# Kernel optimization log

Measured on AMD Instinct MI355X. Metric: run time of the kernel, lower is better.

## Reference

```python
import jax, jax.numpy as jnp
import numpy as np

NUM_CLASSES = 81
THRESHOLD = 0.5
NEGPOS_RATIO = 3
VARIANCE = (0.1, 0.2)


def point_form(p):
    # center-size -> corner form
    return jnp.concatenate([p[:, :2] - p[:, 2:] / 2, p[:, :2] + p[:, 2:] / 2], axis=1)


def jaccard(box_a, box_b):
    # box_a: [O,4] corners, box_b: [P,4] corners -> IoU [O,P]
    lt = jnp.maximum(box_a[:, None, :2], box_b[None, :, :2])
    rb = jnp.minimum(box_a[:, None, 2:], box_b[None, :, 2:])
    wh = jnp.clip(rb - lt, 0.0)
    inter = wh[..., 0] * wh[..., 1]
    area_a = ((box_a[:, 2] - box_a[:, 0]) * (box_a[:, 3] - box_a[:, 1]))[:, None]
    area_b = ((box_b[:, 2] - box_b[:, 0]) * (box_b[:, 3] - box_b[:, 1]))[None, :]
    return inter / (area_a + area_b - inter)


def encode(matched, priors, variances):
    # matched: [P,4] corner GT, priors: [P,4] center-size
    g_cxcy = (matched[:, :2] + matched[:, 2:]) / 2 - priors[:, :2]
    g_cxcy = g_cxcy / (variances[0] * priors[:, 2:])
    g_wh = (matched[:, 2:] - matched[:, :2]) / priors[:, 2:]
    g_wh = jnp.log(g_wh) / variances[1]
    return jnp.concatenate([g_cxcy, g_wh], axis=1)


def match_one(truths, labels, priors):
    overlaps = jaccard(truths, point_form(priors))   # [O,P]
    best_prior_idx = jnp.argmax(overlaps, axis=1)     # [O] best prior per truth
    best_truth_overlap = jnp.max(overlaps, axis=0)    # [P]
    best_truth_idx = jnp.argmax(overlaps, axis=0)     # [P] best truth per prior
    # force each truth's best prior to match that truth
    best_truth_overlap = best_truth_overlap.at[best_prior_idx].set(2.0)
    best_truth_idx = best_truth_idx.at[best_prior_idx].set(jnp.arange(truths.shape[0]))
    matched = truths[best_truth_idx]                  # [P,4]
    conf = labels[best_truth_idx].astype(jnp.int32) + 1
    conf = jnp.where(best_truth_overlap < THRESHOLD, 0, conf)
    loc = encode(matched, priors, VARIANCE)
    return loc, conf


def _loss(loc_data, conf_data, targets, priors):
    B, P, C = conf_data.shape
    loc_t, conf_t = jax.vmap(lambda t: match_one(t[:, :4], t[:, 4], priors))(targets)
    pos = conf_t > 0                                  # [B,P]
    # smooth-L1 (beta=1) over positive priors, sum reduction
    d = loc_data - loc_t
    sl1 = jnp.where(jnp.abs(d) < 1.0, 0.5 * d * d, jnp.abs(d) - 0.5)
    loss_l = jnp.sum(jnp.where(pos[..., None], sl1, 0.0))
    # per-prior CE used both for mining ranking and the final conf loss
    ce = jax.nn.logsumexp(conf_data, axis=-1) - jnp.take_along_axis(
        conf_data, conf_t[..., None], axis=-1)[..., 0]   # [B,P]
    # hard negative mining: zero positives, double argsort for rank
    loss_c_rank = jnp.where(pos, 0.0, ce)
    loss_idx = jnp.argsort(-loss_c_rank, axis=1)
    idx_rank = jnp.argsort(loss_idx, axis=1)
    num_pos = jnp.sum(pos, axis=1, keepdims=True)     # [B,1]
    num_neg = jnp.minimum(NEGPOS_RATIO * num_pos, P - 1)
    neg = idx_rank < num_neg
    sel = pos | neg
    loss_c = jnp.sum(jnp.where(sel, ce, 0.0))
    N = jnp.sum(num_pos).astype(loc_data.dtype)
    return loss_l / N, loss_c / N


def setup_inputs():
    key = jax.random.key(0)
    kl, kc, kb1, kb2, kll, kp1, kp2 = jax.random.split(key, 7)
    B, P, O, C = 64, 8732, 50, NUM_CLASSES
    loc_data = jax.random.normal(kl, (B, P, 4), jnp.float32)
    conf_data = jax.random.normal(kc, (B, P, C), jnp.float32)
    # valid GT boxes in corner form inside [0,1]
    cxcy = jax.random.uniform(kb1, (B, O, 2), minval=0.2, maxval=0.8)
    wh = jax.random.uniform(kb2, (B, O, 2), minval=0.05, maxval=0.3)
    boxes = jnp.concatenate([cxcy - wh / 2, cxcy + wh / 2], axis=-1)
    labels = jax.random.randint(kll, (B, O), 0, C - 1).astype(jnp.float32)
    targets = jnp.concatenate([boxes, labels[..., None]], axis=-1)  # [B,O,5]
    # priors in center-size form
    pcxcy = jax.random.uniform(kp1, (P, 2), minval=0.05, maxval=0.95)
    pwh = jax.random.uniform(kp2, (P, 2), minval=0.05, maxval=0.5)
    priors = jnp.concatenate([pcxcy, pwh], axis=-1)
    return {"loc_data": loc_data, "conf_data": conf_data, "targets": targets, "priors": priors}


def reference(loc_data, conf_data, targets, priors):
    return _loss(loc_data, conf_data, targets, priors)
```

## Files before the change

kernel.cpp:

```cpp
#include <hip/hip_runtime.h>
#include <float.h>

#pragma clang fp contract(off)

typedef unsigned long long ull;
typedef unsigned int u32;

#define THRESH 0.5f
#define PPT 4
#define CE_R 128
#define SEL_T 512
#define ENC_SEG 1024


__device__ __forceinline__ float sl1(float d) {
    float a = fabsf(d);
    return (a < 1.f) ? 0.5f * d * d : a - 0.5f;
}

__global__ __launch_bounds__(256) void k_match(
        const float* __restrict__ targets, const float* __restrict__ priors,
        float* __restrict__ bto, int* __restrict__ bti, int P, int O, int SEG) {
    const int b = blockIdx.y, seg = blockIdx.x;
    __shared__ float4 tbox[128];
    __shared__ float tarea[128];
    const float* trow = targets + (size_t)b * O * 5;
    for (int o = threadIdx.x; o < O; o += blockDim.x) {
        float x1 = trow[o * 5 + 0], y1 = trow[o * 5 + 1];
        float x2 = trow[o * 5 + 2], y2 = trow[o * 5 + 3];
        tbox[o] = make_float4(x1, y1, x2, y2);
        tarea[o] = (x2 - x1) * (y2 - y1);
    }
    __syncthreads();
    const int p0 = seg * SEG;
    float px1[PPT], py1[PPT], px2[PPT], py2[PPT], pa[PPT];
    float bestv[PPT]; int besto[PPT]; int pidx[PPT];
#pragma unroll
    for (int j = 0; j < PPT; j++) {
        int p = p0 + (int)threadIdx.x + j * 256;
        pidx[j] = p; bestv[j] = -1.f; besto[j] = 0;
        if (p < P) {
            float4 pr = ((const float4*)priors)[p];
            px1[j] = pr.x - pr.z / 2.f;
            py1[j] = pr.y - pr.w / 2.f;
            px2[j] = pr.x + pr.z / 2.f;
            py2[j] = pr.y + pr.w / 2.f;
            pa[j] = (px2[j] - px1[j]) * (py2[j] - py1[j]);
        } else {
            px1[j] = 2.f; py1[j] = 2.f; px2[j] = 2.f; py2[j] = 2.f; pa[j] = 1.f;
        }
    }
    for (int o = 0; o < O; o++) {
        float4 t = tbox[o];
        float ta = tarea[o];
#pragma unroll
        for (int j = 0; j < PPT; j++) {
            float lx = fmaxf(t.x, px1[j]), ly = fmaxf(t.y, py1[j]);
            float rx = fminf(t.z, px2[j]), ry = fminf(t.w, py2[j]);
            float wx = fmaxf(rx - lx, 0.f), wy = fmaxf(ry - ly, 0.f);
            float inter = wx * wy;
            float iou = 0.f;
            if (inter > 0.f) iou = inter / (ta + pa[j] - inter);
            if (iou > bestv[j]) { bestv[j] = iou; besto[j] = o; }
        }
    }
#pragma unroll
    for (int j = 0; j < PPT; j++) {
        if (pidx[j] < P) {
            bto[(size_t)b * P + pidx[j]] = bestv[j];
            bti[(size_t)b * P + pidx[j]] = besto[j];
        }
    }
}

__global__ __launch_bounds__(256) void k_tbest(
        const float* __restrict__ targets, const float* __restrict__ priors,
        ull* __restrict__ tbest, int P, int O, int npairs) {
    int g = blockIdx.x * 4 + ((int)threadIdx.x >> 6);
    int lane = threadIdx.x & 63;
    if (g >= npairs) return;
    int OP = (O + 1) >> 1;
    int b = g / OP;
    int o0 = (g % OP) * 2;
    const float* trow = targets + ((size_t)b * O + o0) * 5;
    float ax1 = trow[0], ay1 = trow[1], ax2 = trow[2], ay2 = trow[3];
    float ta0 = (ax2 - ax1) * (ay2 - ay1);
    bool has1 = (o0 + 1) < O;
    float cx1 = 0, cy1 = 0, cx2 = 0, cy2 = 0, ta1 = 1.f;
    if (has1) {
        cx1 = trow[5]; cy1 = trow[6]; cx2 = trow[7]; cy2 = trow[8];
        ta1 = (cx2 - cx1) * (cy2 - cy1);
    }
    ull k0 = 0, k1 = 0;
    for (int p = lane; p < P; p += 64) {
        float4 pr = ((const float4*)priors)[p];
        float bx1 = pr.x - pr.z / 2.f;
        float by1 = pr.y - pr.w / 2.f;
        float bx2 = pr.x + pr.z / 2.f;
        float by2 = pr.y + pr.w / 2.f;
        float pa = (bx2 - bx1) * (by2 - by1);
        u32 np = ~(u32)p;
        {
            float lx = fmaxf(ax1, bx1), ly = fmaxf(ay1, by1);
            float rx = fminf(ax2, bx2), ry = fminf(ay2, by2);
            float wx = fmaxf(rx - lx, 0.f), wy = fmaxf(ry - ly, 0.f);
            float inter = wx * wy;
            float iou = 0.f;
            if (inter > 0.f) iou = inter / (ta0 + pa - inter);
            ull key = ((ull)__float_as_uint(iou) << 32) | np;
            if (key > k0) k0 = key;
        }
        if (has1) {
            float lx = fmaxf(cx1, bx1), ly = fmaxf(cy1, by1);
            float rx = fminf(cx2, bx2), ry = fminf(cy2, by2);
            float wx = fmaxf(rx - lx, 0.f), wy = fmaxf(ry - ly, 0.f);
            float inter = wx * wy;
            float iou = 0.f;
            if (inter > 0.f) iou = inter / (ta1 + pa - inter);
            ull key = ((ull)__float_as_uint(iou) << 32) | np;
            if (key > k1) k1 = key;
        }
    }
    for (int off = 32; off; off >>= 1) {
        ull a = __shfl_xor(k0, off); if (a > k0) k0 = a;
        ull d = __shfl_xor(k1, off); if (d > k1) k1 = d;
    }
    if (lane == 0) {
        tbest[(size_t)b * O + o0] = k0;
        if (has1) tbest[(size_t)b * O + o0 + 1] = k1;
    }
}

__global__ __launch_bounds__(256) void k_encode(
        const float* __restrict__ targets, const float* __restrict__ priors,
        const float* __restrict__ loc_data, const ull* __restrict__ tbest,
        const float* __restrict__ bto, int* __restrict__ conf_t,
        int* __restrict__ num_pos, float* __restrict__ loss_l,
        int P, int O, int SEG) {
    const int b = blockIdx.y, seg = blockIdx.x;
    __shared__ float tr[64 * 5];
    __shared__ int ov[ENC_SEG];
    __shared__ float redf[4]; __shared__ int redi[4];
    const int p0 = seg * SEG;
    const int p1 = min(p0 + SEG, P);
    const float* trow = targets + (size_t)b * O * 5;
    for (int i = threadIdx.x; i < O * 5; i += blockDim.x) tr[i] = trow[i];
    for (int i = threadIdx.x; i < p1 - p0; i += blockDim.x) ov[i] = -1;
    __syncthreads();
    if ((int)threadIdx.x < O) {
        ull tb = tbest[(size_t)b * O + threadIdx.x];
        u32 p = ~(u32)(tb & 0xFFFFFFFFULL);
        if (p >= (u32)P) p = 0;
        if ((int)p >= p0 && (int)p < p1) atomicMax(&ov[p - p0], (int)threadIdx.x);
    }
    __syncthreads();
    float ll = 0.f; int cnt = 0;
    for (int p = p0 + (int)threadIdx.x; p < p1; p += blockDim.x) {
        size_t idx = (size_t)b * P + p;
        int o = conf_t[idx];
        int ovv = ov[p - p0];
        bool forced = ovv >= 0;
        if (forced) o = ovv;
        float ovl = bto[idx];
        int conf = (!forced && ovl < THRESH) ? 0 : ((int)tr[o * 5 + 4] + 1);
        conf_t[idx] = conf;
        if (conf > 0) {
            cnt++;
            float4 pr = ((const float4*)priors)[p];
            float mx1 = tr[o * 5], my1 = tr[o * 5 + 1];
            float mx2 = tr[o * 5 + 2], my2 = tr[o * 5 + 3];
            float gx = ((mx1 + mx2) / 2.f - pr.x) / (0.1f * pr.z);
            float gy = ((my1 + my2) / 2.f - pr.y) / (0.1f * pr.w);
            float gw = logf((mx2 - mx1) / pr.z) / 0.2f;
            float gh = logf((my2 - my1) / pr.w) / 0.2f;
            float4 ld = ((const float4*)loc_data)[idx];
            ll += sl1(ld.x - gx) + sl1(ld.y - gy) + sl1(ld.z - gw) + sl1(ld.w - gh);
        }
    }
    for (int off = 32; off; off >>= 1) {
        ll += __shfl_down(ll, off);
        cnt += __shfl_down(cnt, off);
    }
    int w = threadIdx.x >> 6;
    if ((threadIdx.x & 63) == 0) { redf[w] = ll; redi[w] = cnt; }
    __syncthreads();
    if (threadIdx.x == 0) {
        float l = 0; int c = 0;
        for (int i = 0; i < 4; i++) { l += redf[i]; c += redi[i]; }
        if (c) atomicAdd(&num_pos[b], c);
        atomicAdd(&loss_l[b], l);
    }
}

__global__ __launch_bounds__(256) void k_ce(
        const float* __restrict__ conf, const int* __restrict__ conf_t,
        float* __restrict__ ce, long long BP) {
    __shared__ float s[CE_R * 81];
    long long r0 = (long long)blockIdx.x * CE_R;
    int nrow = (int)min((long long)CE_R, BP - r0);
    int nfl = nrow * 81;
    const float* src = conf + r0 * 81;
    int nv4 = nfl >> 2;
    const float4* s4 = (const float4*)src;
    for (int i = threadIdx.x; i < nv4; i += 256)
        ((float4*)s)[i] = s4[i];
    for (int i = (nv4 << 2) + (int)threadIdx.x; i < nfl; i += 256)
        s[i] = src[i];
    __syncthreads();
    int row = threadIdx.x >> 1;
    int half = threadIdx.x & 1;
    if (row < nrow) {
        const float* rp = s + row * 81;
        int c0 = half * 41;
        int cn = half ? 40 : 41;
        float sum = 0.f;
        for (int j = 0; j < cn; j++) sum += __expf(rp[c0 + j]);
        sum += __shfl_xor(sum, 1);
        if (half == 0) {
            long long r = r0 + row;
            int t = conf_t[r];
            ce[r] = __logf(sum) - rp[t];
        }
    }
}

__global__ __launch_bounds__(SEL_T) void k_select(
        const float* __restrict__ ce, const int* __restrict__ conf_t,
        const int* __restrict__ num_pos, const float* __restrict__ loss_l,
        float* __restrict__ acc, u32* __restrict__ ticket,
        float* __restrict__ out, int P, int B) {
    extern __shared__ u32 sk[];
    __shared__ u32 whist[SEL_T / 64][16];
    __shared__ u32 hist[16];
    __shared__ float redf[SEL_T / 64]; __shared__ u32 redu[SEL_T / 64];
    __shared__ u32 sh_pval; __shared__ int sh_rem;
    const int b = blockIdx.x;
    const size_t base = (size_t)b * P;
    const int lane = threadIdx.x & 63;
    const int w = threadIdx.x >> 6;
    const int NW = SEL_T / 64;

    float ps = 0.f;
    for (int p = threadIdx.x; p < P; p += SEL_T) {
        int c = conf_t[base + p];
        float v = ce[base + p];
        u32 key;
        if (c > 0) { ps += v; key = 0u; }
        else key = __float_as_uint(fmaxf(v, 0.f));
        sk[p] = key;
    }
    for (int off = 32; off; off >>= 1) ps += __shfl_down(ps, off);
    if (lane == 0) redf[w] = ps;
    __syncthreads();
    float pos_sum = 0.f;
    if (threadIdx.x == 0) {
        for (int i = 0; i < NW; i++) pos_sum += redf[i];
    }

    const int np = num_pos[b];
    const int k = min(3 * np, P - 1);
    u32 pval = 0, pmask = 0; int rem = k;
    if (k > 0) {
        for (int shift = 28; shift >= 0; shift -= 4) {
            __syncthreads();
            ull a0 = 0, a1 = 0;
            for (int p = threadIdx.x; p < P; p += SEL_T) {
                u32 key = sk[p];
                if ((key & pmask) == pval) {
                    u32 dig = (key >> shift) & 15u;
                    ull inc = 1ull << ((dig & 7u) * 8u);
                    if (dig < 8u) a0 += inc; else a1 += inc;
                }
            }
            const ull M = 0x00FF00FF00FF00FFull;
            ull e0 = a0 & M, e1 = (a0 >> 8) & M, e2 = a1 & M, e3 = (a1 >> 8) & M;
            for (int off = 32; off; off >>= 1) {
                e0 += __shfl_xor(e0, off);
                e1 += __shfl_xor(e1, off);
                e2 += __shfl_xor(e2, off);
                e3 += __shfl_xor(e3, off);
            }
            if (lane == 0) {
#pragma unroll
                for (int j = 0; j < 4; j++) {
                    whist[w][2 * j]     = (u32)((e0 >> (16 * j)) & 0xFFFF);
                    whist[w][2 * j + 1] = (u32)((e1 >> (16 * j)) & 0xFFFF);
                    whist[w][8 + 2 * j]     = (u32)((e2 >> (16 * j)) & 0xFFFF);
                    whist[w][8 + 2 * j + 1] = (u32)((e3 >> (16 * j)) & 0xFFFF);
                }
            }
            __syncthreads();
            if (threadIdx.x < 16) {
                u32 h = 0;
                for (int i = 0; i < NW; i++) h += whist[i][threadIdx.x];
                hist[threadIdx.x] = h;
            }
            __syncthreads();
            if (threadIdx.x == 0) {
                u32 accu = 0; int d = 15;
                for (; d > 0; d--) {
                    u32 h = hist[d];
                    if (accu + h >= (u32)rem) break;
                    accu += h;
                }
                sh_pval = pval | ((u32)d << shift);
                sh_rem = rem - (int)accu;
            }
            __syncthreads();
            pval = sh_pval; rem = sh_rem; pmask |= (0xFu << shift);
        }
    }

    float sgt = 0.f; u32 cgt = 0;
    if (k > 0) {
        for (int p = threadIdx.x; p < P; p += SEL_T) {
            u32 key = sk[p];
            if (key > pval) { sgt += __uint_as_float(key); cgt++; }
        }
    }
    for (int off = 32; off; off >>= 1) {
        sgt += __shfl_down(sgt, off);
        cgt += __shfl_down(cgt, off);
    }
    __syncthreads();
    if (lane == 0) { redf[w] = sgt; redu[w] = cgt; }
    __syncthreads();
    if (threadIdx.x == 0) {
        float s = 0.f; u32 c = 0;
        for (int i = 0; i < NW; i++) { s += redf[i]; c += redu[i]; }
        float t = __uint_as_float(pval);
        float lc_b = pos_sum + ((k > 0) ? (s + (float)(k - (int)c) * t) : 0.f);
        atomicAdd(&acc[0], (float)np);
        atomicAdd(&acc[1], loss_l[b]);
        atomicAdd(&acc[2], lc_b);
        __threadfence();
        u32 tk = atomicAdd(ticket, 1u);
        if (tk == (u32)(B - 1)) {
            float n  = atomicAdd(&acc[0], 0.f);
            float ll = atomicAdd(&acc[1], 0.f);
            float lc = atomicAdd(&acc[2], 0.f);
            out[0] = ll / n;
            out[1] = lc / n;
        }
    }
}


extern "C" void kernel_launch(void* const* d_in, const int* in_sizes, int n_in,
                              void* d_out, int out_size, void* d_ws, size_t ws_size,
                              hipStream_t stream) {
    const float* loc     = (const float*)d_in[0];
    const float* conf    = (const float*)d_in[1];
    const float* targets = (const float*)d_in[2];
    const float* priors  = (const float*)d_in[3];

    const int P = in_sizes[3] / 4;
    const int B = in_sizes[0] / (P * 4);
    const int O = in_sizes[2] / (B * 5);

    char* ws = (char*)d_ws;
    size_t off = 0;
    int*   num_pos = (int*)(ws + off);   off += (size_t)B * sizeof(int);
    float* loss_l  = (float*)(ws + off); off += (size_t)B * sizeof(float);
    float* acc     = (float*)(ws + off); off += 4 * sizeof(float);
    u32*   ticket  = (u32*)(ws + off);   off += sizeof(u32);
    const size_t zbytes = off;
    off = (off + 7) & ~(size_t)7;
    ull*   tbest   = (ull*)(ws + off);   off += (size_t)B * O * sizeof(ull);
    float* F       = (float*)(ws + off); off += (size_t)B * P * sizeof(float);
    int*   I       = (int*)(ws + off);   off += (size_t)B * P * sizeof(int);

    (void)hipMemsetAsync(d_ws, 0, zbytes, stream);

    const int SEG = 256 * PPT;
    const int S = (P + SEG - 1) / SEG;
    k_match<<<dim3(S, B), 256, 0, stream>>>(targets, priors, F, I, P, O, SEG);

    const int npairs = B * ((O + 1) / 2);
    k_tbest<<<(npairs + 3) / 4, 256, 0, stream>>>(targets, priors, tbest, P, O, npairs);

    const int S2 = (P + ENC_SEG - 1) / ENC_SEG;
    const int SEG2 = (P + S2 - 1) / S2;
    k_encode<<<dim3(S2, B), 256, 0, stream>>>(targets, priors, loc, tbest, F, I,
                                              num_pos, loss_l, P, O, SEG2);

    const long long BP = (long long)B * P;
    k_ce<<<(int)((BP + CE_R - 1) / CE_R), 256, 0, stream>>>(conf, I, F, BP);

    k_select<<<B, SEL_T, (size_t)P * sizeof(u32), stream>>>(F, I, num_pos, loss_l,
                                                            acc, ticket, (float*)d_out, P, B);
}
```

Before: 402.8 us.

## Fuse match/tbest kernels and encode/CE kernels, drop memset launch

Merges the per-prior match and per-truth best-prior kernels into one launch partitioned by block index, and folds the workspace zeroing into block 0 instead of a separate memset. Encode and cross-entropy are fused so each block computes conf_t into shared memory and then streams its slice of conf_data to compute CE, avoiding a re-read of conf_t and two launches. The fused CE block now uses much more shared memory (about 41KB+8KB), which may reduce occupancy for the bandwidth-heavy conf_data pass. There is also a fixed ENC_SEG segmentation with fewer blocks (9x64) doing CE versus many small blocks before.

```diff
diff --git a/kernel.cpp b/kernel.cpp
--- a/kernel.cpp
+++ b/kernel.cpp
@@ -18,134 +18,142 @@
     return (a < 1.f) ? 0.5f * d * d : a - 0.5f;
 }
 
-__global__ __launch_bounds__(256) void k_match(
+__global__ __launch_bounds__(256) void k_prep(
         const float* __restrict__ targets, const float* __restrict__ priors,
-        float* __restrict__ bto, int* __restrict__ bti, int P, int O, int SEG) {
-    const int b = blockIdx.y, seg = blockIdx.x;
+        float* __restrict__ bto, int* __restrict__ bti, ull* __restrict__ tbest,
+        u32* __restrict__ zws, int nz,
+        int P, int O, int S, int SB, int npairs) {
+    const int bid = blockIdx.x;
     __shared__ float4 tbox[128];
     __shared__ float tarea[128];
-    const float* trow = targets + (size_t)b * O * 5;
-    for (int o = threadIdx.x; o < O; o += blockDim.x) {
-        float x1 = trow[o * 5 + 0], y1 = trow[o * 5 + 1];
-        float x2 = trow[o * 5 + 2], y2 = trow[o * 5 + 3];
-        tbox[o] = make_float4(x1, y1, x2, y2);
-        tarea[o] = (x2 - x1) * (y2 - y1);
-    }
-    __syncthreads();
-    const int p0 = seg * SEG;
-    float px1[PPT], py1[PPT], px2[PPT], py2[PPT], pa[PPT];
-    float bestv[PPT]; int besto[PPT]; int pidx[PPT];
-#pragma unroll
-    for (int j = 0; j < PPT; j++) {
-        int p = p0 + (int)threadIdx.x + j * 256;
-        pidx[j] = p; bestv[j] = -1.f; besto[j] = 0;
-        if (p < P) {
-            float4 pr = ((const float4*)priors)[p];
-            px1[j] = pr.x - pr.z / 2.f;
-            py1[j] = pr.y - pr.w / 2.f;
-            px2[j] = pr.x + pr.z / 2.f;
-            py2[j] = pr.y + pr.w / 2.f;
-            pa[j] = (px2[j] - px1[j]) * (py2[j] - py1[j]);
-        } else {
-            px1[j] = 2.f; py1[j] = 2.f; px2[j] = 2.f; py2[j] = 2.f; pa[j] = 1.f;
-        }
-    }
-    for (int o = 0; o < O; o++) {
-        float4 t = tbox[o];
-        float ta = tarea[o];
+    if (bid < SB) {
+        if (bid == 0)
+            for (int i = threadIdx.x; i < nz; i += 256) zws[i] = 0;
+        const int b = bid / S, seg = bid % S;
+        const float* trow = targets + (size_t)b * O * 5;
+        for (int o = threadIdx.x; o < O; o += 256) {
+            float x1 = trow[o * 5 + 0], y1 = trow[o * 5 + 1];
+            float x2 = trow[o * 5 + 2], y2 = trow[o * 5 + 3];
+            tbox[o] = make_float4(x1, y1, x2, y2);
+            tarea[o] = (x2 - x1) * (y2 - y1);
+        }
+        __syncthreads();
+        const int p0 = seg * (256 * PPT);
+        float px1[PPT], py1[PPT], px2[PPT], py2[PPT], pa[PPT];
+        float bestv[PPT]; int besto[PPT]; int pidx[PPT];
 #pragma unroll
         for (int j = 0; j < PPT; j++) {
-            float lx = fmaxf(t.x, px1[j]), ly = fmaxf(t.y, py1[j]);
-            float rx = fminf(t.z, px2[j]), ry = fminf(t.w, py2[j]);
-            float wx = fmaxf(rx - lx, 0.f), wy = fmaxf(ry - ly, 0.f);
-            float inter = wx * wy;
-            float iou = 0.f;
-            if (inter > 0.f) iou = inter / (ta + pa[j] - inter);
-            if (iou > bestv[j]) { bestv[j] = iou; besto[j] = o; }
-        }
-    }
+            int p = p0 + (int)threadIdx.x + j * 256;
+            pidx[j] = p; bestv[j] = -1.f; besto[j] = 0;
+            if (p < P) {
+                float4 pr = ((const float4*)priors)[p];
+                px1[j] = pr.x - pr.z / 2.f;
+                py1[j] = pr.y - pr.w / 2.f;
+                px2[j] = pr.x + pr.z / 2.f;
+                py2[j] = pr.y + pr.w / 2.f;
+                pa[j] = (px2[j] - px1[j]) * (py2[j] - py1[j]);
+            } else {
+                px1[j] = 2.f; py1[j] = 2.f; px2[j] = 2.f; py2[j] = 2.f; pa[j] = 1.f;
+            }
+        }
+        for (int o = 0; o < O; o++) {
+            float4 t = tbox[o];
+            float ta = tarea[o];
 #pragma unroll
-    for (int j = 0; j < PPT; j++) {
-        if (pidx[j] < P) {
-            bto[(size_t)b * P + pidx[j]] = bestv[j];
-            bti[(size_t)b * P + pidx[j]] = besto[j];
-        }
-    }
-}
-
-__global__ __launch_bounds__(256) void k_tbest(
+            for (int j = 0; j < PPT; j++) {
+                float lx = fmaxf(t.x, px1[j]), ly = fmaxf(t.y, py1[j]);
+                float rx = fminf(t.z, px2[j]), ry = fminf(t.w, py2[j]);
+                float wx = fmaxf(rx - lx, 0.f), wy = fmaxf(ry - ly, 0.f);
+                float inter = wx * wy;
+                float iou = 0.f;
+                if (inter > 0.f) iou = inter / (ta + pa[j] - inter);
+                if (iou > bestv[j]) { bestv[j] = iou; besto[j] = o; }
+            }
+        }
+#pragma unroll
+        for (int j = 0; j < PPT; j++) {
+            if (pidx[j] < P) {
+                bto[(size_t)b * P + pidx[j]] = bestv[j];
+                bti[(size_t)b * P + pidx[j]] = besto[j];
+            }
+        }
+    } else {
+        int g = (bid - SB) * 4 + ((int)threadIdx.x >> 6);
+        int lane = threadIdx.x & 63;
+        if (g >= npairs) return;
+        int OP = (O + 1) >> 1;
+        int b = g / OP;
+        int o0 = (g % OP) * 2;
+        const float* trow = targets + ((size_t)b * O + o0) * 5;
+        float ax1 = trow[0], ay1 = trow[1], ax2 = trow[2], ay2 = trow[3];
+        float ta0 = (ax2 - ax1) * (ay2 - ay1);
+        bool has1 = (o0 + 1) < O;
+        float cx1 = 0, cy1 = 0, cx2 = 0, cy2 = 0, ta1 = 1.f;
+        if (has1) {
+            cx1 = trow[5]; cy1 = trow[6]; cx2 = trow[7]; cy2 = trow[8];
+            ta1 = (cx2 - cx1) * (cy2 - cy1);
+        }
+        ull k0 = 0, k1 = 0;
+        for (int p = lane; p < P; p += 64) {
+            float4 pr = ((const float4*)priors)[p];
+            float bx1 = pr.x - pr.z / 2.f;
+            float by1 = pr.y - pr.w / 2.f;
+            float bx2 = pr.x + pr.z / 2.f;
+            float by2 = pr.y + pr.w / 2.f;
+            float pa = (bx2 - bx1) * (by2 - by1);
+            u32 np = ~(u32)p;
+            {
+                float lx = fmaxf(ax1, bx1), ly = fmaxf(ay1, by1);
+                float rx = fminf(ax2, bx2), ry = fminf(ay2, by2);
+                float wx = fmaxf(rx - lx, 0.f), wy = fmaxf(ry - ly, 0.f);
+                float inter = wx * wy;
+                float iou = 0.f;
+                if (inter > 0.f) iou = inter / (ta0 + pa - inter);
+                ull key = ((ull)__float_as_uint(iou) << 32) | np;
+                if (key > k0) k0 = key;
+            }
+            if (has1) {
+                float lx = fmaxf(cx1, bx1), ly = fmaxf(cy1, by1);
+                float rx = fminf(cx2, bx2), ry = fminf(cy2, by2);
+                float wx = fmaxf(rx - lx, 0.f), wy = fmaxf(ry - ly, 0.f);
+                float inter = wx * wy;
+                float iou = 0.f;
+                if (inter > 0.f) iou = inter / (ta1 + pa - inter);
+                ull key = ((ull)__float_as_uint(iou) << 32) | np;
+                if (key > k1) k1 = key;
+            }
+        }
+        for (int off = 32; off; off >>= 1) {
+            ull a = __shfl_xor(k0, off); if (a > k0) k0 = a;
+            ull d = __shfl_xor(k1, off); if (d > k1) k1 = d;
+        }
+        if (lane == 0) {
+            tbest[(size_t)b * O + o0] = k0;
+            if (has1) tbest[(size_t)b * O + o0 + 1] = k1;
+        }
+    }
+}
+
+__global__ __launch_bounds__(256) void k_encode_ce(
         const float* __restrict__ targets, const float* __restrict__ priors,
-        ull* __restrict__ tbest, int P, int O, int npairs) {
-    int g = blockIdx.x * 4 + ((int)threadIdx.x >> 6);
-    int lane = threadIdx.x & 63;
-    if (g >= npairs) return;
-    int OP = (O + 1) >> 1;
-    int b = g / OP;
-    int o0 = (g % OP) * 2;
-    const float* trow = targets + ((size_t)b * O + o0) * 5;
-    float ax1 = trow[0], ay1 = trow[1], ax2 = trow[2], ay2 = trow[3];
-    float ta0 = (ax2 - ax1) * (ay2 - ay1);
-    bool has1 = (o0 + 1) < O;
-    float cx1 = 0, cy1 = 0, cx2 = 0, cy2 = 0, ta1 = 1.f;
-    if (has1) {
-        cx1 = trow[5]; cy1 = trow[6]; cx2 = trow[7]; cy2 = trow[8];
-        ta1 = (cx2 - cx1) * (cy2 - cy1);
-    }
-    ull k0 = 0, k1 = 0;
-    for (int p = lane; p < P; p += 64) {
-        float4 pr = ((const float4*)priors)[p];
-        float bx1 = pr.x - pr.z / 2.f;
-        float by1 = pr.y - pr.w / 2.f;
-        float bx2 = pr.x + pr.z / 2.f;
-        float by2 = pr.y + pr.w / 2.f;
-        float pa = (bx2 - bx1) * (by2 - by1);
-        u32 np = ~(u32)p;
-        {
-            float lx = fmaxf(ax1, bx1), ly = fmaxf(ay1, by1);
-            float rx = fminf(ax2, bx2), ry = fminf(ay2, by2);
-            float wx = fmaxf(rx - lx, 0.f), wy = fmaxf(ry - ly, 0.f);
-            float inter = wx * wy;
-            float iou = 0.f;
-            if (inter > 0.f) iou = inter / (ta0 + pa - inter);
-            ull key = ((ull)__float_as_uint(iou) << 32) | np;
-            if (key > k0) k0 = key;
-        }
-        if (has1) {
-            float lx = fmaxf(cx1, bx1), ly = fmaxf(cy1, by1);
-            float rx = fminf(cx2, bx2), ry = fminf(cy2, by2);
-            float wx = fmaxf(rx - lx, 0.f), wy = fmaxf(ry - ly, 0.f);
-            float inter = wx * wy;
-            float iou = 0.f;
-            if (inter > 0.f) iou = inter / (ta1 + pa - inter);
-            ull key = ((ull)__float_as_uint(iou) << 32) | np;
-            if (key > k1) k1 = key;
-        }
-    }
-    for (int off = 32; off; off >>= 1) {
-        ull a = __shfl_xor(k0, off); if (a > k0) k0 = a;
-        ull d = __shfl_xor(k1, off); if (d > k1) k1 = d;
-    }
-    if (lane == 0) {
-        tbest[(size_t)b * O + o0] = k0;
-        if (has1) tbest[(size_t)b * O + o0 + 1] = k1;
-    }
-}
-
-__global__ __launch_bounds__(256) void k_encode(
-        const float* __restrict__ targets, const float* __restrict__ priors,
-        const float* __restrict__ loc_data, const ull* __restrict__ tbest,
-        const float* __restrict__ bto, int* __restrict__ conf_t,
+        const float* __restrict__ loc_data, const float* __restrict__ conf,
+        const ull* __restrict__ tbest,
+        float* __restrict__ F,
+        int* __restrict__ conf_t,
         int* __restrict__ num_pos, float* __restrict__ loss_l,
-        int P, int O, int SEG) {
+        int P, int O) {
     const int b = blockIdx.y, seg = blockIdx.x;
     __shared__ float tr[64 * 5];
     __shared__ int ov[ENC_SEG];
+    __shared__ int ct[ENC_SEG];
+    __shared__ float s[CE_R * 81];
     __shared__ float redf[4]; __shared__ int redi[4];
-    const int p0 = seg * SEG;
-    const int p1 = min(p0 + SEG, P);
+    const int p0 = seg * ENC_SEG;
+    const int p1 = min(p0 + ENC_SEG, P);
+    const int nprior = p1 - p0;
     const float* trow = targets + (size_t)b * O * 5;
-    for (int i = threadIdx.x; i < O * 5; i += blockDim.x) tr[i] = trow[i];
-    for (int i = threadIdx.x; i < p1 - p0; i += blockDim.x) ov[i] = -1;
+    for (int i = threadIdx.x; i < O * 5; i += 256) tr[i] = trow[i];
+    for (int i = threadIdx.x; i < nprior; i += 256) ov[i] = -1;
     __syncthreads();
     if ((int)threadIdx.x < O) {
         ull tb = tbest[(size_t)b * O + threadIdx.x];
@@ -155,16 +163,17 @@
     }
     __syncthreads();
     float ll = 0.f; int cnt = 0;
-    for (int p = p0 + (int)threadIdx.x; p < p1; p += blockDim.x) {
+    for (int p = p0 + (int)threadIdx.x; p < p1; p += 256) {
         size_t idx = (size_t)b * P + p;
         int o = conf_t[idx];
         int ovv = ov[p - p0];
         bool forced = ovv >= 0;
         if (forced) o = ovv;
-        float ovl = bto[idx];
-        int conf = (!forced && ovl < THRESH) ? 0 : ((int)tr[o * 5 + 4] + 1);
-        conf_t[idx] = conf;
-        if (conf > 0) {
+        float ovl = F[idx];
+        int cv = (!forced && ovl < THRESH) ? 0 : ((int)tr[o * 5 + 4] + 1);
+        conf_t[idx] = cv;
+        ct[p - p0] = cv;
+        if (cv > 0) {
             cnt++;
             float4 pr = ((const float4*)priors)[p];
             float mx1 = tr[o * 5], my1 = tr[o * 5 + 1];
@@ -190,36 +199,30 @@
         if (c) atomicAdd(&num_pos[b], c);
         atomicAdd(&loss_l[b], l);
     }
-}
-
-__global__ __launch_bounds__(256) void k_ce(
-        const float* __restrict__ conf, const int* __restrict__ conf_t,
-        float* __restrict__ ce, long long BP) {
-    __shared__ float s[CE_R * 81];
-    long long r0 = (long long)blockIdx.x * CE_R;
-    int nrow = (int)min((long long)CE_R, BP - r0);
-    int nfl = nrow * 81;
-    const float* src = conf + r0 * 81;
-    int nv4 = nfl >> 2;
-    const float4* s4 = (const float4*)src;
-    for (int i = threadIdx.x; i < nv4; i += 256)
-        ((float4*)s)[i] = s4[i];
-    for (int i = (nv4 << 2) + (int)threadIdx.x; i < nfl; i += 256)
-        s[i] = src[i];
-    __syncthreads();
-    int row = threadIdx.x >> 1;
-    int half = threadIdx.x & 1;
-    if (row < nrow) {
-        const float* rp = s + row * 81;
-        int c0 = half * 41;
-        int cn = half ? 40 : 41;
-        float sum = 0.f;
-        for (int j = 0; j < cn; j++) sum += __expf(rp[c0 + j]);
-        sum += __shfl_xor(sum, 1);
-        if (half == 0) {
-            long long r = r0 + row;
-            int t = conf_t[r];
-            ce[r] = __logf(sum) - rp[t];
+    for (int c0 = 0; c0 < nprior; c0 += CE_R) {
+        __syncthreads();
+        int nrow = min(CE_R, nprior - c0);
+        int nfl = nrow * 81;
+        const float* src = conf + ((size_t)b * P + p0 + c0) * 81;
+        int nv4 = nfl >> 2;
+        for (int i = threadIdx.x; i < nv4; i += 256)
+            ((float4*)s)[i] = ((const float4*)src)[i];
+        for (int i = (nv4 << 2) + (int)threadIdx.x; i < nfl; i += 256)
+            s[i] = src[i];
+        __syncthreads();
+        int row = threadIdx.x >> 1;
+        int half = threadIdx.x & 1;
+        if (row < nrow) {
+            const float* rp = s + row * 81;
+            int cc0 = half * 41;
+            int cn = half ? 40 : 41;
+            float sum = 0.f;
+            for (int j = 0; j < cn; j++) sum += __expf(rp[cc0 + j]);
+            sum += __shfl_xor(sum, 1);
+            if (half == 0) {
+                int t = ct[c0 + row];
+                F[(size_t)b * P + p0 + c0 + row] = __logf(sum) - rp[t];
+            }
         }
     }
 }
@@ -364,28 +367,23 @@
     float* loss_l  = (float*)(ws + off); off += (size_t)B * sizeof(float);
     float* acc     = (float*)(ws + off); off += 4 * sizeof(float);
     u32*   ticket  = (u32*)(ws + off);   off += sizeof(u32);
-    const size_t zbytes = off;
+    const int zwords = (int)(off >> 2);
     off = (off + 7) & ~(size_t)7;
     ull*   tbest   = (ull*)(ws + off);   off += (size_t)B * O * sizeof(ull);
     float* F       = (float*)(ws + off); off += (size_t)B * P * sizeof(float);
     int*   I       = (int*)(ws + off);   off += (size_t)B * P * sizeof(int);
 
-    (void)hipMemsetAsync(d_ws, 0, zbytes, stream);
-
     const int SEG = 256 * PPT;
     const int S = (P + SEG - 1) / SEG;
-    k_match<<<dim3(S, B), 256, 0, stream>>>(targets, priors, F, I, P, O, SEG);
-
+    const int SB = S * B;
     const int npairs = B * ((O + 1) / 2);
-    k_tbest<<<(npairs + 3) / 4, 256, 0, stream>>>(targets, priors, tbest, P, O, npairs);
+    const int TB = (npairs + 3) / 4;
+    k_prep<<<SB + TB, 256, 0, stream>>>(targets, priors, F, I, tbest,
+                                        (u32*)ws, zwords, P, O, S, SB, npairs);
 
     const int S2 = (P + ENC_SEG - 1) / ENC_SEG;
-    const int SEG2 = (P + S2 - 1) / S2;
-    k_encode<<<dim3(S2, B), 256, 0, stream>>>(targets, priors, loc, tbest, F, I,
-                                              num_pos, loss_l, P, O, SEG2);
-
-    const long long BP = (long long)B * P;
-    k_ce<<<(int)((BP + CE_R - 1) / CE_R), 256, 0, stream>>>(conf, I, F, BP);
+    k_encode_ce<<<dim3(S2, B), 256, 0, stream>>>(targets, priors, loc, conf, tbest,
+                                                 F, I, num_pos, loss_l, P, O);
 
     k_select<<<B, SEL_T, (size_t)P * sizeof(u32), stream>>>(F, I, num_pos, loss_l,
                                                             acc, ticket, (float*)d_out, P, B);
```

New measurement: 386.8 us. 4.0% less time.
